# Performance work log

Hardware: AMD Instinct MI355X
Metric: run time of the kernel (lower is better)

The kernel has to match this reference:

```python
import jax, jax.numpy as jnp
import numpy as np

D_MODEL = 512
D_STATE = 64
LN_EPS = 1e-3  # Keras LayerNormalization default epsilon


def setup_inputs() -> dict:
    key = jax.random.key(0)
    ks = jax.random.split(key, 12)
    B, S, D, N = 8, 4096, D_MODEL, D_STATE

    def glorot(k, shape):
        fan_in, fan_out = shape[0], shape[1]
        lim = np.sqrt(6.0 / (fan_in + fan_out)).astype(np.float32)
        return jax.random.uniform(k, shape, jnp.float32, -lim, lim)

    return {
        "x": jax.random.normal(ks[0], (B, S, D), jnp.float32),
        "ln_gamma": jnp.ones((D,), jnp.float32),
        "ln_beta": jnp.zeros((D,), jnp.float32),
        "W_in": glorot(ks[1], (D, D)),
        "b_in": jnp.zeros((D,), jnp.float32),
        "W_xs": glorot(ks[2], (D, N)),
        "W_B": glorot(ks[3], (D, N)),
        "b_B": jnp.zeros((N,), jnp.float32),
        "W_C": glorot(ks[4], (D, N)),
        "b_C": jnp.zeros((N,), jnp.float32),
        "A_log": jax.random.uniform(ks[5], (N,), jnp.float32, -4.0, -1.0),
        "D_skip": jnp.ones((D,), jnp.float32),
        "W_so": glorot(ks[6], (N, D)),
        "W_out": glorot(ks[7], (D, D)),
        "b_out": jnp.zeros((D,), jnp.float32),
    }


def reference(x, ln_gamma, ln_beta, W_in, b_in, W_xs, W_B, b_B, W_C, b_C,
              A_log, D_skip, W_so, W_out, b_out):
    residual = x
    # LayerNorm over last axis (Keras default eps=1e-3)
    mu = jnp.mean(x, axis=-1, keepdims=True)
    var = jnp.mean(jnp.square(x - mu), axis=-1, keepdims=True)
    xn = (x - mu) * jax.lax.rsqrt(var + LN_EPS) * ln_gamma + ln_beta
    # input projection (this projected x is what feeds the D skip too)
    xp = xn @ W_in + b_in                      # [B, S, D]
    Bmat = xp @ W_B + b_B                      # [B, S, N] selective B(x)
    Cmat = xp @ W_C + b_C                      # [B, S, N] selective C(x)
    xs = xp @ W_xs                             # [B, S, N]
    A_bar = jnp.exp(-jnp.exp(A_log))           # [N], stable decay in (0,1)
    Bx = Bmat * xs                             # per-step drive B_t * x_state_t

    # sequential scan: h_t = A_bar * h_{t-1} + Bx_t
    def step(h, bx):
        h = A_bar * h + bx
        return h, h

    h0 = jnp.zeros((x.shape[0], A_log.shape[0]), x.dtype)
    _, hs = jax.lax.scan(step, h0, jnp.swapaxes(Bx, 0, 1))  # hs: [S, B, N]
    hs = jnp.swapaxes(hs, 0, 1)                             # [B, S, N]

    y = jnp.einsum('bsn,nd->bsd', Cmat * hs, W_so) + D_skip * xp
    y = y @ W_out + b_out
    # dropout is identity at inference (training=None)
    return y + residual
```

## Files before the change

kernel.cpp:

```cpp
#include <hip/hip_runtime.h>
#include <cstdint>
#include <cstddef>


typedef unsigned short bf16_t;
typedef __attribute__((ext_vector_type(8))) short bh8;
typedef __attribute__((ext_vector_type(4))) float f4;

#define M_ROWS 32768
#define SCAN_L 16
#define SCAN_C 256

__device__ __forceinline__ unsigned short f2bf(float f) {
  union { float f; unsigned int u; } c; c.f = f;
  unsigned int u = c.u;
  return (unsigned short)((u + 0x7FFFu + ((u >> 16) & 1u)) >> 16);
}

__device__ __forceinline__ uint2 pack4bf(f4 a) {
  uint2 r;
  r.x = (unsigned)f2bf(a[0]) | ((unsigned)f2bf(a[1]) << 16);
  r.y = (unsigned)f2bf(a[2]) | ((unsigned)f2bf(a[3]) << 16);
  return r;
}

__device__ __forceinline__ void async_cp16(void* lds, const void* g) {
  __builtin_amdgcn_global_load_lds((const __attribute__((address_space(1))) void*)g,
                                   (__attribute__((address_space(3))) void*)lds, 16, 0, 0);
}

__global__ __launch_bounds__(256) void prep_all(
    const float* __restrict__ W_in, const float* __restrict__ W_out,
    const float* __restrict__ W_so, const float* __restrict__ W_xs,
    const float* __restrict__ W_B,  const float* __restrict__ W_C,
    const float* __restrict__ b_in, const float* __restrict__ D_skip,
    const float* __restrict__ A_log,
    bf16_t* __restrict__ Wout_t, bf16_t* __restrict__ Wdout_t,
    bf16_t* __restrict__ Win_b, bf16_t* __restrict__ Wso_b,
    bf16_t* __restrict__ Wcat_t, bf16_t* __restrict__ Wproj,
    float* __restrict__ Abar, float* __restrict__ Apow) {
  int i = blockIdx.x * 256 + threadIdx.x;
  if (i < 262144) { int k = i >> 9, n = i & 511;
    Wout_t[(size_t)n * 512 + k] = f2bf(W_out[k * 512 + n]); return; }
  i -= 262144;
  if (i < 262144) { int k = i >> 9, n = i & 511;
    Wdout_t[(size_t)n * 512 + k] = f2bf(D_skip[k] * W_out[k * 512 + n]); return; }
  i -= 262144;
  if (i < 262144) { Win_b[i] = f2bf(W_in[i]); return; }
  i -= 262144;
  if (i < 65536) { int r = i >> 9, j = i & 511;
    Win_b[(size_t)(512 + r) * 512 + j] = (r == 0) ? f2bf(b_in[j]) : (bf16_t)0; return; }
  i -= 65536;
  if (i < 65536) { int k = i >> 9, j = i & 511;
    Wso_b[i] = (k < 64) ? f2bf(W_so[k * 512 + j]) : (bf16_t)0; return; }
  i -= 65536;
  if (i < 131072) { int k = i >> 8, n = i & 255;
    float v = 0.f;
    if (n < 128) { int g = n >> 5, w = n & 31;
      v = (w < 16) ? W_xs[k * 64 + g * 16 + w] : W_B[k * 64 + g * 16 + (w - 16)];
    } else if (n < 192) v = W_C[k * 64 + n - 128];
    Wcat_t[(size_t)n * 512 + k] = f2bf(v); return; }
  i -= 131072;
  if (i < 32768) { int r = i >> 9, d = i & 511;
    Wproj[(size_t)(192 + r) * 512 + d] = 0; return; }
  i -= 32768;
  if (i < 64) {
    float a = __expf(A_log[i]);
    Abar[i] = __expf(-a);
    Apow[i] = __expf(-a * (float)SCAN_L);
  }
}

__global__ __launch_bounds__(256, 4) void prep2_fused(
    const bf16_t* __restrict__ Win_b, const bf16_t* __restrict__ Wcat_t,
    const bf16_t* __restrict__ Wso_b, const bf16_t* __restrict__ Wout_t,
    const bf16_t* __restrict__ Wdout_t,
    const float* __restrict__ b_B, const float* __restrict__ b_C,
    bf16_t* __restrict__ Wproj, bf16_t* __restrict__ Wcat2,
    float* __restrict__ biasp, float* __restrict__ biasW2,
    const float* __restrict__ x, const float* __restrict__ gamma,
    const float* __restrict__ beta, bf16_t* __restrict__ xn) {
  __shared__ __align__(16) bf16_t As[128 * 64];
  __shared__ __align__(16) bf16_t Bs[128 * 64];
  const int tid = threadIdx.x;

  if (blockIdx.x >= 34) {
    const int row = (int)(blockIdx.x - 34) * 4 + (tid >> 6);
    const int lane = tid & 63;
    const float* xr = x + (size_t)row * 512 + lane * 8;
    float4 v0 = *(const float4*)xr;
    float4 v1 = *(const float4*)(xr + 4);
    float s  = v0.x + v0.y + v0.z + v0.w + v1.x + v1.y + v1.z + v1.w;
    float sq = v0.x*v0.x + v0.y*v0.y + v0.z*v0.z + v0.w*v0.w
             + v1.x*v1.x + v1.y*v1.y + v1.z*v1.z + v1.w*v1.w;
    #pragma unroll
    for (int off = 32; off > 0; off >>= 1) {
      s  += __shfl_xor(s, off, 64);
      sq += __shfl_xor(sq, off, 64);
    }
    const float mu  = s * (1.0f / 512.0f);
    const float var = sq * (1.0f / 512.0f) - mu * mu;
    const float rs  = rsqrtf(var + 1e-3f);
    float4 g0 = *(const float4*)(gamma + lane * 8);
    float4 g1 = *(const float4*)(gamma + lane * 8 + 4);
    float4 b0 = *(const float4*)(beta + lane * 8);
    float4 b1 = *(const float4*)(beta + lane * 8 + 4);
    bh8 ov;
    ov[0] = (short)f2bf((v0.x - mu) * rs * g0.x + b0.x);
    ov[1] = (short)f2bf((v0.y - mu) * rs * g0.y + b0.y);
    ov[2] = (short)f2bf((v0.z - mu) * rs * g0.z + b0.z);
    ov[3] = (short)f2bf((v0.w - mu) * rs * g0.w + b0.w);
    ov[4] = (short)f2bf((v1.x - mu) * rs * g1.x + b1.x);
    ov[5] = (short)f2bf((v1.y - mu) * rs * g1.y + b1.y);
    ov[6] = (short)f2bf((v1.z - mu) * rs * g1.z + b1.z);
    ov[7] = (short)f2bf((v1.w - mu) * rs * g1.w + b1.w);
    *(bh8*)(xn + (size_t)row * 512 + lane * 8) = ov;
    return;
  }

  const int bx = blockIdx.x;
  const int wave = tid >> 6, lane = tid & 63;
  const int quad = lane >> 4, l16 = lane & 15;
  const int wm = (wave >> 1) * 64, wn = (wave & 1) * 64;
  int role, mb, nb;
  if (bx < 10)      { role = 0; mb = bx >> 1; nb = bx & 1; }
  else if (bx < 14) { role = 1; mb = 0; nb = bx - 10; }
  else { role = 2; int t = bx - 14; mb = t >> 2; nb = t & 3; }
  const bf16_t* Ap = (role == 1) ? Wso_b : Win_b;
  const bf16_t* Bp = (role == 0) ? Wcat_t : (role == 1) ? Wout_t : Wdout_t;

  f4 acc[4][4];
  #pragma unroll
  for (int i = 0; i < 4; ++i)
    #pragma unroll
    for (int j = 0; j < 4; ++j) acc[i][j] = (f4){0.f, 0.f, 0.f, 0.f};

  for (int kt = 0; kt < 8; ++kt) {
    const int k0 = kt << 6;
    __syncthreads();
    #pragma unroll
    for (int i = 0; i < 4; ++i) {
      const int base = (wave * 4 + i) * 64;
      const int cid = base + lane;
      const int row = cid >> 3;
      const int g = (cid & 7) ^ (row & 7);
      async_cp16((char*)As + base * 16,
                 Ap + (size_t)(mb * 128 + row) * 512 + k0 + g * 8);
    }
    #pragma unroll
    for (int i = 0; i < 4; ++i) {
      const int base = (wave * 4 + i) * 64;
      const int cid = base + lane;
      const int row = cid >> 3;
      const int g = (cid & 7) ^ (row & 7);
      async_cp16((char*)Bs + base * 16,
                 Bp + (size_t)(nb * 128 + row) * 512 + k0 + g * 8);
    }
    __syncthreads();
    #pragma unroll
    for (int ks = 0; ks < 2; ++ks) {
      const int gb = ks * 4 + quad;
      bh8 af[4], bfv[4];
      #pragma unroll
      for (int im = 0; im < 4; ++im) {
        const int row = wm + im * 16 + l16;
        af[im] = *(const bh8*)((const char*)As + row * 128 + ((gb ^ (row & 7)) * 16));
      }
      #pragma unroll
      for (int in_ = 0; in_ < 4; ++in_) {
        const int row = wn + in_ * 16 + l16;
        bfv[in_] = *(const bh8*)((const char*)Bs + row * 128 + ((gb ^ (row & 7)) * 16));
      }
      #pragma unroll
      for (int im = 0; im < 4; ++im)
        #pragma unroll
        for (int in_ = 0; in_ < 4; ++in_)
          acc[im][in_] = __builtin_amdgcn_mfma_f32_16x16x32_bf16(af[im], bfv[in_],
                                                                 acc[im][in_], 0, 0, 0);
    }
  }

  #pragma unroll
  for (int im = 0; im < 4; ++im) {
    #pragma unroll
    for (int in_ = 0; in_ < 4; ++in_) {
      const int row0 = mb * 128 + wm + im * 16 + quad * 4;
      const int col = nb * 128 + wn + in_ * 16 + l16;
      if (role == 0) {
        if (col < 192) {
          if (row0 < 512) {
            *(uint2*)(Wproj + (size_t)col * 512 + row0) = pack4bf(acc[im][in_]);
          } else if (row0 == 512) {
            float v = acc[im][in_][0];
            if (col < 128) { int w = col & 31;
              if (w >= 16) v += b_B[(col >> 5) * 16 + (w - 16)];
            } else v += b_C[col - 128];
            biasp[col] = v;
          }
        }
      } else if (role == 1) {
        if (row0 < 64)
          *(uint2*)(Wcat2 + (size_t)col * 576 + row0) = pack4bf(acc[im][in_]);
      } else {
        if (row0 < 512) {
          *(uint2*)(Wcat2 + (size_t)col * 576 + 64 + row0) = pack4bf(acc[im][in_]);
        } else if (row0 == 512) {
          biasW2[col] = acc[im][in_][0];
        }
      }
    }
  }
}

__global__ __launch_bounds__(256, 4) void gemm_proj(
    const bf16_t* __restrict__ A0, const bf16_t* __restrict__ Wt,
    float* __restrict__ outf, const float* __restrict__ bias1,
    const float* __restrict__ Abar, float* __restrict__ carryT) {
  __shared__ __align__(16) char smem[32768];
  bf16_t* As = (bf16_t*)smem;
  bf16_t* Bs = (bf16_t*)(smem + 16384);
  const int tid = threadIdx.x;
  const int wave = tid >> 6, lane = tid & 63;
  const int quad = lane >> 4, l16 = lane & 15;
  const int wm = (wave >> 1) * 64, wn = (wave & 1) * 64;
  const int mb = blockIdx.x, nb = blockIdx.y;
  const int K = 512;

  f4 acc[4][4];
  #pragma unroll
  for (int i = 0; i < 4; ++i)
    #pragma unroll
    for (int j = 0; j < 4; ++j) acc[i][j] = (f4){0.f, 0.f, 0.f, 0.f};

  for (int kt = 0; kt < 8; ++kt) {
    const int k0 = kt << 6;
    __syncthreads();
    #pragma unroll
    for (int i = 0; i < 4; ++i) {
      const int base = (wave * 4 + i) * 64;
      const int cid = base + lane;
      const int row = cid >> 3;
      const int g = (cid & 7) ^ (row & 7);
      async_cp16((char*)As + base * 16,
                 A0 + (size_t)(mb * 128 + row) * K + k0 + g * 8);
    }
    #pragma unroll
    for (int i = 0; i < 4; ++i) {
      const int base = (wave * 4 + i) * 64;
      const int cid = base + lane;
      const int row = cid >> 3;
      const int g = (cid & 7) ^ (row & 7);
      async_cp16((char*)Bs + base * 16,
                 Wt + (size_t)(nb * 128 + row) * K + k0 + g * 8);
    }
    __syncthreads();

    #pragma unroll
    for (int ks = 0; ks < 2; ++ks) {
      const int gb = ks * 4 + quad;
      bh8 af[4], bfv[4];
      #pragma unroll
      for (int im = 0; im < 4; ++im) {
        const int row = wm + im * 16 + l16;
        af[im] = *(const bh8*)((const char*)As + row * 128 + ((gb ^ (row & 7)) * 16));
      }
      #pragma unroll
      for (int in_ = 0; in_ < 4; ++in_) {
        const int row = wn + in_ * 16 + l16;
        bfv[in_] = *(const bh8*)((const char*)Bs + row * 128 + ((gb ^ (row & 7)) * 16));
      }
      #pragma unroll
      for (int im = 0; im < 4; ++im)
        #pragma unroll
        for (int in_ = 0; in_ < 4; ++in_)
          acc[im][in_] = __builtin_amdgcn_mfma_f32_16x16x32_bf16(af[im], bfv[in_],
                                                                 acc[im][in_], 0, 0, 0);
    }
  }

  __syncthreads();
  float* lt = (float*)smem;

  if (nb == 0) {
    float* wb = lt + wave * 2048;
    #pragma unroll
    for (int im = 0; im < 4; ++im)
      #pragma unroll
      for (int pp = 0; pp < 2; ++pp)
        #pragma unroll
        for (int r = 0; r < 4; ++r) {
          const int c0 = wn + (2 * pp) * 16 + l16;
          const float vx = acc[im][2 * pp][r]     + bias1[c0];
          const float vb = acc[im][2 * pp + 1][r] + bias1[c0 + 16];
          wb[(im * 16 + quad * 4 + r) * 32 + pp * 16 + l16] = vx * vb;
        }
    const int rsub = lane >> 3, cg8 = lane & 7;
    #pragma unroll
    for (int rr = 0; rr < 8; ++rr) {
      const int rl = rr * 8 + rsub;
      f4 v = *(f4*)(wb + rl * 32 + cg8 * 4);
      const size_t row = (size_t)(mb * 128 + wm + rl);
      *(f4*)(outf + row * 64 + (wn >> 1) + cg8 * 4) = v;
    }
    {
      const int bb = mb >> 5;
      const int cbase = (mb & 31) * 8 + (wm >> 4);
      const int ch = lane & 31;
      const int n = (wn >> 1) + ch;
      const float A = Abar[n];
      #pragma unroll
      for (int t = 0; t < 2; ++t) {
        const int cl = (lane >> 5) + 2 * t;
        float hv = 0.f;
        #pragma unroll
        for (int i = 0; i < SCAN_L; ++i)
          hv = fmaf(A, hv, wb[(cl * SCAN_L + i) * 32 + ch]);
        carryT[(size_t)(cbase + cl) * 512 + bb * 64 + n] = hv;
      }
    }
  } else if (wn == 0) {
    float* wb = lt + (wave >> 1) * 4096;
    #pragma unroll
    for (int im = 0; im < 4; ++im)
      #pragma unroll
      for (int in_ = 0; in_ < 4; ++in_)
        #pragma unroll
        for (int r = 0; r < 4; ++r) {
          const int c = in_ * 16 + l16;
          wb[(im * 16 + quad * 4 + r) * 64 + c] = acc[im][in_][r] + bias1[128 + c];
        }
    #pragma unroll
    for (int rr = 0; rr < 16; ++rr) {
      const int rl = rr * 4 + quad;
      f4 v = *(f4*)(wb + rl * 64 + l16 * 4);
      const size_t row = (size_t)(mb * 128 + wm + rl);
      *(f4*)(outf + ((size_t)M_ROWS + row) * 64 + l16 * 4) = v;
    }
  }
}

__global__ __launch_bounds__(256, 6) void gemm_out(
    const bf16_t* __restrict__ CH, const bf16_t* __restrict__ xn,
    const bf16_t* __restrict__ Wt, float* __restrict__ outf,
    const float* __restrict__ bias0, const float* __restrict__ bias1,
    const float* __restrict__ resid) {
  __shared__ __align__(16) bf16_t As[64 * 64];
  __shared__ __align__(16) bf16_t Bs[128 * 64];
  const int tid = threadIdx.x;
  const int wave = tid >> 6, lane = tid & 63;
  const int quad = lane >> 4, l16 = lane & 15;
  const int wm = (wave >> 1) * 32, wn = (wave & 1) * 64;
  const int mb = blockIdx.x, nb = blockIdx.y;
  const int K = 576;

  f4 acc[2][4];
  #pragma unroll
  for (int i = 0; i < 2; ++i)
    #pragma unroll
    for (int j = 0; j < 4; ++j) acc[i][j] = (f4){0.f, 0.f, 0.f, 0.f};

  for (int kt = 0; kt < 9; ++kt) {
    const int k0 = kt << 6;
    const bf16_t* Ap; int lda, kk;
    if (kt == 0) { Ap = CH; lda = 64;  kk = 0; }
    else         { Ap = xn; lda = 512; kk = k0 - 64; }

    __syncthreads();
    #pragma unroll
    for (int i = 0; i < 2; ++i) {
      const int base = (wave * 2 + i) * 64;
      const int cid = base + lane;
      const int row = cid >> 3;
      const int g = (cid & 7) ^ (row & 7);
      async_cp16((char*)As + base * 16,
                 Ap + (size_t)(mb * 64 + row) * lda + kk + g * 8);
    }
    #pragma unroll
    for (int i = 0; i < 4; ++i) {
      const int base = (wave * 4 + i) * 64;
      const int cid = base + lane;
      const int row = cid >> 3;
      const int g = (cid & 7) ^ (row & 7);
      async_cp16((char*)Bs + base * 16,
                 Wt + (size_t)(nb * 128 + row) * K + k0 + g * 8);
    }
    __syncthreads();

    #pragma unroll
    for (int ks = 0; ks < 2; ++ks) {
      const int gb = ks * 4 + quad;
      bh8 af[2], bfv[4];
      #pragma unroll
      for (int im = 0; im < 2; ++im) {
        const int row = wm + im * 16 + l16;
        af[im] = *(const bh8*)((const char*)As + row * 128 + ((gb ^ (row & 7)) * 16));
      }
      #pragma unroll
      for (int in_ = 0; in_ < 4; ++in_) {
        const int row = wn + in_ * 16 + l16;
        bfv[in_] = *(const bh8*)((const char*)Bs + row * 128 + ((gb ^ (row & 7)) * 16));
      }
      #pragma unroll
      for (int im = 0; im < 2; ++im)
        #pragma unroll
        for (int in_ = 0; in_ < 4; ++in_)
          acc[im][in_] = __builtin_amdgcn_mfma_f32_16x16x32_bf16(af[im], bfv[in_],
                                                                 acc[im][in_], 0, 0, 0);
    }
  }

  #pragma unroll
  for (int im = 0; im < 2; ++im) {
    #pragma unroll
    for (int in_ = 0; in_ < 4; ++in_) {
      const int col = nb * 128 + wn + in_ * 16 + l16;
      const float bsum = bias0[col] + bias1[col];
      #pragma unroll
      for (int r = 0; r < 4; ++r) {
        const int row = mb * 64 + wm + im * 16 + quad * 4 + r;
        const size_t idx = (size_t)row * 512 + col;
        outf[idx] = acc[im][in_][r] + bsum + resid[idx];
      }
    }
  }
}

__global__ __launch_bounds__(64) void scan_apply(
    const float* __restrict__ projP, const float* __restrict__ Abar,
    const float* __restrict__ Apow, const float* __restrict__ carryT,
    bf16_t* __restrict__ CH) {
  const int b = blockIdx.x >> 8, c = blockIdx.x & (SCAN_C - 1), n = threadIdx.x;
  const float A = Abar[n];
  const float Ap = Apow[n];
  const float Ap4 = (Ap * Ap) * (Ap * Ap);
  const float* cr = carryT + b * 64 + n;
  float h0 = 0.f, h1 = 0.f, h2 = 0.f, h3 = 0.f;
  int j = 0;
  for (; j + 4 <= c; j += 4) {
    h0 = fmaf(Ap4, h0, cr[(size_t)j * 512]);
    h1 = fmaf(Ap4, h1, cr[(size_t)(j + 1) * 512]);
    h2 = fmaf(Ap4, h2, cr[(size_t)(j + 2) * 512]);
    h3 = fmaf(Ap4, h3, cr[(size_t)(j + 3) * 512]);
  }
  float h = fmaf(Ap, fmaf(Ap, fmaf(Ap, h0, h1), h2), h3);
  for (; j < c; ++j) h = fmaf(Ap, h, cr[(size_t)j * 512]);
  const size_t row0 = (size_t)b * 4096 + c * SCAN_L;
  const float* pBx = projP + row0 * 64;
  const float* pC  = projP + ((size_t)M_ROWS + row0) * 64;
  bf16_t* o = CH + row0 * 64;
  for (int i = 0; i < SCAN_L; ++i) {
    h = fmaf(A, h, pBx[i * 64 + n]);
    o[i * 64 + n] = f2bf(pC[i * 64 + n] * h);
  }
}

extern "C" void kernel_launch(void* const* d_in, const int* in_sizes, int n_in,
                              void* d_out, int out_size, void* d_ws, size_t ws_size,
                              hipStream_t stream) {
  const float* x      = (const float*)d_in[0];
  const float* ln_g   = (const float*)d_in[1];
  const float* ln_b   = (const float*)d_in[2];
  const float* W_in   = (const float*)d_in[3];
  const float* b_in   = (const float*)d_in[4];
  const float* W_xs   = (const float*)d_in[5];
  const float* W_B    = (const float*)d_in[6];
  const float* b_B    = (const float*)d_in[7];
  const float* W_C    = (const float*)d_in[8];
  const float* b_C    = (const float*)d_in[9];
  const float* A_log  = (const float*)d_in[10];
  const float* D_skip = (const float*)d_in[11];
  const float* W_so   = (const float*)d_in[12];
  const float* W_out  = (const float*)d_in[13];
  const float* b_out  = (const float*)d_in[14];
  float* out = (float*)d_out;

  char* w = (char*)d_ws;
  auto carve = [&](size_t bytes) {
    char* p = w; w += (bytes + 255) & ~(size_t)255; return p;
  };
  bf16_t* xn     = (bf16_t*)carve((size_t)M_ROWS * 512 * 2);
  float*  projP  = (float*)carve((size_t)2 * M_ROWS * 64 * 4);
  bf16_t* CH     = (bf16_t*)carve((size_t)M_ROWS * 64 * 2);
  float*  carryT = (float*)carve((size_t)SCAN_C * 512 * 4);
  bf16_t* Wproj  = (bf16_t*)carve((size_t)256 * 512 * 2);
  bf16_t* Wcat2  = (bf16_t*)carve((size_t)512 * 576 * 2);
  bf16_t* Win_b  = (bf16_t*)carve((size_t)640 * 512 * 2);
  bf16_t* Wso_b  = (bf16_t*)carve((size_t)128 * 512 * 2);
  bf16_t* Wout_t = (bf16_t*)carve((size_t)512 * 512 * 2);
  bf16_t* Wdout_t= (bf16_t*)carve((size_t)512 * 512 * 2);
  bf16_t* Wcat_t = (bf16_t*)carve((size_t)256 * 512 * 2);
  float*  biasp  = (float*)carve(192 * 4);
  float*  biasW2 = (float*)carve(512 * 4);
  float*  Abar   = (float*)carve(256);
  float*  Apow   = (float*)carve(256);

  prep_all<<<4227, 256, 0, stream>>>(W_in, W_out, W_so, W_xs, W_B, W_C, b_in,
                                     D_skip, A_log, Wout_t, Wdout_t, Win_b,
                                     Wso_b, Wcat_t, Wproj, Abar, Apow);
  prep2_fused<<<34 + 8192, 256, 0, stream>>>(Win_b, Wcat_t, Wso_b, Wout_t,
                                             Wdout_t, b_B, b_C, Wproj, Wcat2,
                                             biasp, biasW2, x, ln_g, ln_b, xn);
  gemm_proj<<<dim3(256, 2), 256, 0, stream>>>(xn, Wproj, projP, biasp,
                                              Abar, carryT);
  scan_apply<<<8 * SCAN_C, 64, 0, stream>>>(projP, Abar, Apow, carryT, CH);
  gemm_out<<<dim3(512, 4), 256, 0, stream>>>(CH, xn, Wcat2, out,
                                             b_out, biasW2, x);
}
```

Before: 219.5 us.

## Fuse scan apply into output GEMM prologue, writing scan results to LDS

```diff
diff --git a/kernel.cpp b/kernel.cpp
--- a/kernel.cpp
+++ b/kernel.cpp
@@ -339,9 +339,11 @@
   }
 }
 
-__global__ __launch_bounds__(256, 6) void gemm_out(
-    const bf16_t* __restrict__ CH, const bf16_t* __restrict__ xn,
-    const bf16_t* __restrict__ Wt, float* __restrict__ outf,
+__global__ __launch_bounds__(256, 4) void gemm_out(
+    const float* __restrict__ projP, const float* __restrict__ Abar,
+    const float* __restrict__ Apow, const float* __restrict__ carryT,
+    const bf16_t* __restrict__ xn, const bf16_t* __restrict__ Wt,
+    float* __restrict__ outf,
     const float* __restrict__ bias0, const float* __restrict__ bias1,
     const float* __restrict__ resid) {
   __shared__ __align__(16) bf16_t As[64 * 64];
@@ -353,6 +355,39 @@
   const int mb = blockIdx.x, nb = blockIdx.y;
   const int K = 576;
 
+  {
+    const int n = lane;
+    const int cl = wave;
+    const int bb = mb >> 6;
+    const int c0 = (mb & 63) * 4 + cl;
+    const float A = Abar[n];
+    const float Ap = Apow[n];
+    const float Ap4 = (Ap * Ap) * (Ap * Ap);
+    const float* cr = carryT + bb * 64 + n;
+    float h0 = 0.f, h1 = 0.f, h2 = 0.f, h3 = 0.f;
+    int j = 0;
+    for (; j + 4 <= c0; j += 4) {
+      h0 = fmaf(Ap4, h0, cr[(size_t)j * 512]);
+      h1 = fmaf(Ap4, h1, cr[(size_t)(j + 1) * 512]);
+      h2 = fmaf(Ap4, h2, cr[(size_t)(j + 2) * 512]);
+      h3 = fmaf(Ap4, h3, cr[(size_t)(j + 3) * 512]);
+    }
+    float h = fmaf(Ap, fmaf(Ap, fmaf(Ap, h0, h1), h2), h3);
+    for (; j < c0; ++j) h = fmaf(Ap, h, cr[(size_t)j * 512]);
+    const size_t row0 = (size_t)mb * 64 + cl * 16;
+    const float* pBx = projP + row0 * 64;
+    const float* pC  = projP + ((size_t)M_ROWS + row0) * 64;
+    char* asb = (char*)As;
+    const int g = n >> 3, boff = (n & 7) * 2;
+    #pragma unroll
+    for (int i = 0; i < SCAN_L; ++i) {
+      h = fmaf(A, h, pBx[i * 64 + n]);
+      const int row = cl * 16 + i;
+      *(bf16_t*)(asb + row * 128 + ((g ^ (row & 7)) * 16) + boff) =
+          f2bf(pC[i * 64 + n] * h);
+    }
+  }
+
   f4 acc[2][4];
   #pragma unroll
   for (int i = 0; i < 2; ++i)
@@ -361,19 +396,17 @@
 
   for (int kt = 0; kt < 9; ++kt) {
     const int k0 = kt << 6;
-    const bf16_t* Ap; int lda, kk;
-    if (kt == 0) { Ap = CH; lda = 64;  kk = 0; }
-    else         { Ap = xn; lda = 512; kk = k0 - 64; }
-
     __syncthreads();
-    #pragma unroll
-    for (int i = 0; i < 2; ++i) {
-      const int base = (wave * 2 + i) * 64;
-      const int cid = base + lane;
-      const int row = cid >> 3;
-      const int g = (cid & 7) ^ (row & 7);
-      async_cp16((char*)As + base * 16,
-                 Ap + (size_t)(mb * 64 + row) * lda + kk + g * 8);
+    if (kt > 0) {
+      #pragma unroll
+      for (int i = 0; i < 2; ++i) {
+        const int base = (wave * 2 + i) * 64;
+        const int cid = base + lane;
+        const int row = cid >> 3;
+        const int g = (cid & 7) ^ (row & 7);
+        async_cp16((char*)As + base * 16,
+                   xn + (size_t)(mb * 64 + row) * 512 + (k0 - 64) + g * 8);
+      }
     }
     #pragma unroll
     for (int i = 0; i < 4; ++i) {
@@ -422,35 +455,6 @@
         outf[idx] = acc[im][in_][r] + bsum + resid[idx];
       }
     }
-  }
-}
-
-__global__ __launch_bounds__(64) void scan_apply(
-    const float* __restrict__ projP, const float* __restrict__ Abar,
-    const float* __restrict__ Apow, const float* __restrict__ carryT,
-    bf16_t* __restrict__ CH) {
-  const int b = blockIdx.x >> 8, c = blockIdx.x & (SCAN_C - 1), n = threadIdx.x;
-  const float A = Abar[n];
-  const float Ap = Apow[n];
-  const float Ap4 = (Ap * Ap) * (Ap * Ap);
-  const float* cr = carryT + b * 64 + n;
-  float h0 = 0.f, h1 = 0.f, h2 = 0.f, h3 = 0.f;
-  int j = 0;
-  for (; j + 4 <= c; j += 4) {
-    h0 = fmaf(Ap4, h0, cr[(size_t)j * 512]);
-    h1 = fmaf(Ap4, h1, cr[(size_t)(j + 1) * 512]);
-    h2 = fmaf(Ap4, h2, cr[(size_t)(j + 2) * 512]);
-    h3 = fmaf(Ap4, h3, cr[(size_t)(j + 3) * 512]);
-  }
-  float h = fmaf(Ap, fmaf(Ap, fmaf(Ap, h0, h1), h2), h3);
-  for (; j < c; ++j) h = fmaf(Ap, h, cr[(size_t)j * 512]);
-  const size_t row0 = (size_t)b * 4096 + c * SCAN_L;
-  const float* pBx = projP + row0 * 64;
-  const float* pC  = projP + ((size_t)M_ROWS + row0) * 64;
-  bf16_t* o = CH + row0 * 64;
-  for (int i = 0; i < SCAN_L; ++i) {
-    h = fmaf(A, h, pBx[i * 64 + n]);
-    o[i * 64 + n] = f2bf(pC[i * 64 + n] * h);
   }
 }
 
@@ -480,7 +484,6 @@
   };
   bf16_t* xn     = (bf16_t*)carve((size_t)M_ROWS * 512 * 2);
   float*  projP  = (float*)carve((size_t)2 * M_ROWS * 64 * 4);
-  bf16_t* CH     = (bf16_t*)carve((size_t)M_ROWS * 64 * 2);
   float*  carryT = (float*)carve((size_t)SCAN_C * 512 * 4);
   bf16_t* Wproj  = (bf16_t*)carve((size_t)256 * 512 * 2);
   bf16_t* Wcat2  = (bf16_t*)carve((size_t)512 * 576 * 2);
@@ -502,7 +505,7 @@
                                              biasp, biasW2, x, ln_g, ln_b, xn);
   gemm_proj<<<dim3(256, 2), 256, 0, stream>>>(xn, Wproj, projP, biasp,
                                               Abar, carryT);
-  scan_apply<<<8 * SCAN_C, 64, 0, stream>>>(projP, Abar, Apow, carryT, CH);
-  gemm_out<<<dim3(512, 4), 256, 0, stream>>>(CH, xn, Wcat2, out,
+  gemm_out<<<dim3(512, 4), 256, 0, stream>>>(projP, Abar, Apow, carryT,
+                                             xn, Wcat2, out,
                                              b_out, biasW2, x);
 }
```

Measured after the change: 219.1 us. About the same (-0.2%).
